# Optimization experiments

Hardware: AMD Instinct MI355X
Metric: run time of the kernel (lower is better)

Reference implementation:

```python
import jax, jax.numpy as jnp
import numpy as np

N_NODES = 100000
N_FEAT = 256
OUT_DIM = 128
NNZ_X = 1_600_000
NNZ_A = 1_600_000
DROPOUT = 0.0  # layer default; floor(1-p+u) mask is all-ones -> deterministic


def setup_inputs() -> dict:
    key = jax.random.key(0)
    k = jax.random.split(key, 7)
    feat_rows = jax.random.randint(k[0], (NNZ_X,), 0, N_NODES, dtype=jnp.int32)
    feat_cols = jax.random.randint(k[1], (NNZ_X,), 0, N_FEAT, dtype=jnp.int32)
    feat_vals = jax.random.normal(k[2], (NNZ_X,), dtype=jnp.float32)
    adj_rows = jax.random.randint(k[3], (NNZ_A,), 0, N_NODES, dtype=jnp.int32)
    adj_cols = jax.random.randint(k[4], (NNZ_A,), 0, N_NODES, dtype=jnp.int32)
    adj_vals = jax.random.uniform(k[5], (NNZ_A,), dtype=jnp.float32)
    glorot_std = np.sqrt(2.0 / (N_FEAT + OUT_DIM)).astype(np.float32)
    W = jax.random.normal(k[6], (N_FEAT, OUT_DIM), dtype=jnp.float32) * glorot_std
    return {
        "feat_rows": feat_rows, "feat_cols": feat_cols, "feat_vals": feat_vals,
        "adj_rows": adj_rows, "adj_cols": adj_cols, "adj_vals": adj_vals,
        "W": W, "n_nodes": N_NODES,
    }


def reference(feat_rows, feat_cols, feat_vals, adj_rows, adj_cols, adj_vals, W, n_nodes):
    # sparse dropout on feature nonzeros: mask = floor((1-p) + uniform) in {0,1}
    u = jax.random.uniform(jax.random.key(1), feat_vals.shape, dtype=feat_vals.dtype)
    keep = jnp.floor((1.0 - DROPOUT) + u)
    vals = feat_vals * keep * (1.0 / (1.0 - DROPOUT))
    # X @ W : gather W rows by feature column, scale by nnz value, scatter-add into node rows
    xw = jax.ops.segment_sum(vals[:, None] * W[feat_cols], feat_rows,
                             num_segments=n_nodes)  # [N, D]
    # A @ (X @ W) : gather node rows by edge source, scale by edge weight, scatter-add to dest
    agg = jax.ops.segment_sum(adj_vals[:, None] * xw[adj_cols], adj_rows,
                              num_segments=n_nodes)  # [N, D]
    return jax.nn.relu(agg)
```

## Files before the change

### kernel.cpp

```cpp
#include <hip/hip_runtime.h>
#include <hip/hip_fp16.h>

#define OUT_DIM 128
#define NPS 256
#define NS_MAX 400
#define CAP_S 4608
#define EPT2 18
#define SBLK1 256
#define EPT1 16
#define CHUNK1 (SBLK1 * EPT1)
#define SBLK2 256
#define GBLK 256

__global__ __launch_bounds__(SBLK1) void scatter1_kernel(
    const int* __restrict__ adj_rows, const int* __restrict__ adj_cols,
    const float* __restrict__ adj_vals, int nnz_a, int nCkA,
    const int* __restrict__ feat_rows, const int* __restrict__ feat_cols,
    const float* __restrict__ feat_vals, int nnz_x,
    int* __restrict__ cur, int2* __restrict__ pay, int ns)
{
    __shared__ int2 s_stage[CHUNK1];
    __shared__ unsigned short s_bin[CHUNK1];
    __shared__ int s_hist[NS_MAX];
    __shared__ int s_excl[NS_MAX];
    __shared__ int s_gbase[NS_MAX];

    int tid = threadIdx.x;
    bool isA = ((int)blockIdx.x < nCkA);
    const int* rows; const int* cols; const float* vals;
    int nnz, start, matbase;
    if (isA) {
        rows = adj_rows; cols = adj_cols; vals = adj_vals; nnz = nnz_a;
        start = (int)blockIdx.x * CHUNK1; matbase = 0;
    } else {
        rows = feat_rows; cols = feat_cols; vals = feat_vals; nnz = nnz_x;
        start = ((int)blockIdx.x - nCkA) * CHUNK1; matbase = ns;
    }
    int total = nnz - start; if (total > CHUNK1) total = CHUNK1;

    for (int i = tid; i < ns; i += SBLK1) s_hist[i] = 0;
    __syncthreads();

    int rr[EPT1]; int cc[EPT1]; float vv[EPT1];
    #pragma unroll
    for (int k = 0; k < EPT1; ++k) {
        int e = start + k * SBLK1 + tid;
        rr[k] = -1;
        if (e < nnz) {
            rr[k] = rows[e]; cc[k] = cols[e]; vv[k] = vals[e];
            atomicAdd(&s_hist[rr[k] >> 8], 1);
        }
    }
    __syncthreads();

    if (tid < 64) {
        int carry = 0;
        for (int seg = 0; seg < ns; seg += 64) {
            int idx = seg + tid;
            int x = (idx < ns) ? s_hist[idx] : 0;
            int incl = x;
            #pragma unroll
            for (int off = 1; off < 64; off <<= 1) {
                int y = __shfl_up(incl, off, 64);
                if (tid >= off) incl += y;
            }
            if (idx < ns) s_excl[idx] = carry + incl - x;
            carry += __shfl(incl, 63, 64);
        }
    }
    __syncthreads();

    for (int i = tid; i < ns; i += SBLK1) {
        int c = s_hist[i];
        s_gbase[i] = (c > 0) ? atomicAdd(&cur[matbase + i], c) : 0;
        s_hist[i] = 0;
    }
    __syncthreads();

    #pragma unroll
    for (int k = 0; k < EPT1; ++k) {
        if (rr[k] >= 0) {
            int b = rr[k] >> 8;
            int rl = rr[k] & 255;
            int pos = s_excl[b] + atomicAdd(&s_hist[b], 1);
            s_stage[pos] = make_int2((rl << 17) | cc[k], __float_as_int(vv[k]));
            s_bin[pos] = (unsigned short)b;
        }
    }
    __syncthreads();

    for (int i = tid; i < total; i += SBLK1) {
        int b = s_bin[i];
        int g = s_gbase[b] + (i - s_excl[b]);
        if (g < CAP_S)
            pay[(size_t)(matbase + b) * CAP_S + g] = s_stage[i];
    }
}

__global__ __launch_bounds__(SBLK2) void sort2_kernel(
    const int* __restrict__ cur, int2* __restrict__ pay,
    int2* __restrict__ row_span, int ns, int n_nodes)
{
    __shared__ int s_cnt[NPS];
    __shared__ int s_excl[NPS];
    int b = blockIdx.x;
    int tid = threadIdx.x;
    int count = cur[b]; if (count > CAP_S) count = CAP_S;
    int2* region = pay + (size_t)b * CAP_S;

    s_cnt[tid] = 0;
    __syncthreads();

    int2 er[EPT2];
    #pragma unroll
    for (int k = 0; k < EPT2; ++k) {
        int i = tid + k * SBLK2;
        er[k] = make_int2(-1, 0);
        if (i < count) {
            er[k] = region[i];
            atomicAdd(&s_cnt[((unsigned)er[k].x) >> 17], 1);
        }
    }
    __syncthreads();

    if (tid < 64) {
        int carry = 0;
        #pragma unroll
        for (int seg = 0; seg < NPS; seg += 64) {
            int x = s_cnt[seg + tid];
            int incl = x;
            #pragma unroll
            for (int off = 1; off < 64; off <<= 1) {
                int y = __shfl_up(incl, off, 64);
                if (tid >= off) incl += y;
            }
            s_excl[seg + tid] = carry + incl - x;
            carry += __shfl(incl, 63, 64);
        }
    }
    __syncthreads();

    int m = (b >= ns) ? 1 : 0;
    int g = (b - m * ns) * NPS + tid;
    if (g < n_nodes)
        row_span[(size_t)m * n_nodes + g] = make_int2(b * CAP_S + s_excl[tid], s_cnt[tid]);
    __syncthreads();

    #pragma unroll
    for (int k = 0; k < EPT2; ++k) {
        if (er[k].x >= 0) {
            int rl = ((unsigned)er[k].x) >> 17;
            int pos = atomicAdd(&s_excl[rl], 1);
            region[pos] = make_int2(er[k].x & 0x1FFFF, er[k].y);
        }
    }
}

__global__ __launch_bounds__(GBLK) void gather_xw_kernel(
    const int2* __restrict__ row_span, const int2* __restrict__ pay,
    const float* __restrict__ W, __half* __restrict__ XW, int n_nodes)
{
    int tid = threadIdx.x;
    int lane = tid & 15;
    int node = blockIdx.x * 16 + (tid >> 4);
    if (node >= n_nodes) return;
    int2 span = row_span[(size_t)n_nodes + node];
    int s = span.x, cnt = span.y;
    const float4* Wv = (const float4*)W;
    float a0=0,a1=0,a2=0,a3=0,a4=0,a5=0,a6=0,a7=0;
    for (int base = 0; base < cnt; base += 16) {
        int mm = cnt - base; if (mm > 16) mm = 16;
        int2 pl = make_int2(0, 0);
        if (lane < mm) pl = pay[s + base + lane];
        #pragma unroll 4
        for (int j = 0; j < mm; ++j) {
            int c = __shfl(pl.x, j, 16);
            float v = __int_as_float(__shfl(pl.y, j, 16));
            float4 f0 = Wv[c * 32 + lane * 2];
            float4 f1 = Wv[c * 32 + lane * 2 + 1];
            a0 += v * f0.x; a1 += v * f0.y; a2 += v * f0.z; a3 += v * f0.w;
            a4 += v * f1.x; a5 += v * f1.y; a6 += v * f1.z; a7 += v * f1.w;
        }
    }
    union { int4 i4; __half2 h[4]; } o;
    o.h[0] = __floats2half2_rn(a0, a1);
    o.h[1] = __floats2half2_rn(a2, a3);
    o.h[2] = __floats2half2_rn(a4, a5);
    o.h[3] = __floats2half2_rn(a6, a7);
    ((int4*)(XW + (size_t)node * OUT_DIM))[lane] = o.i4;
}

__global__ __launch_bounds__(GBLK, 4) void gather_agg_kernel(
    const int2* __restrict__ row_span, const int2* __restrict__ pay,
    const __half* __restrict__ XW, float* __restrict__ out, int n_nodes)
{
    int tid = threadIdx.x;
    int lane = tid & 15;
    int node = blockIdx.x * 16 + (tid >> 4);
    if (node >= n_nodes) return;
    int2 span = row_span[node];
    int s = span.x, cnt = span.y;
    const int4* Xv = (const int4*)XW;
    float a0=0,a1=0,a2=0,a3=0,a4=0,a5=0,a6=0,a7=0;
    int2 pl = make_int2(0, 0);
    if (lane < cnt) pl = pay[s + lane];
    for (int base = 0; base < cnt; base += 16) {
        int4 w[16];
        #pragma unroll
        for (int j = 0; j < 16; ++j) {
            int c = __shfl(pl.x, j, 16);
            w[j] = Xv[(size_t)((c << 4) | lane)];
        }
        int2 pln = make_int2(0, 0);
        if (base + 16 + lane < cnt) pln = pay[s + base + 16 + lane];
        #pragma unroll
        for (int j = 0; j < 16; ++j) {
            float v = __int_as_float(__shfl(pl.y, j, 16));
            union { int4 i4; __half2 h[4]; } u;
            u.i4 = w[j];
            float2 f0 = __half22float2(u.h[0]);
            float2 f1 = __half22float2(u.h[1]);
            float2 f2 = __half22float2(u.h[2]);
            float2 f3 = __half22float2(u.h[3]);
            a0 += v * f0.x; a1 += v * f0.y; a2 += v * f1.x; a3 += v * f1.y;
            a4 += v * f2.x; a5 += v * f2.y; a6 += v * f3.x; a7 += v * f3.y;
        }
        pl = pln;
    }
    float4 lo, hi;
    lo.x = fmaxf(a0, 0.f); lo.y = fmaxf(a1, 0.f);
    lo.z = fmaxf(a2, 0.f); lo.w = fmaxf(a3, 0.f);
    hi.x = fmaxf(a4, 0.f); hi.y = fmaxf(a5, 0.f);
    hi.z = fmaxf(a6, 0.f); hi.w = fmaxf(a7, 0.f);
    float4* orow = (float4*)(out + (size_t)node * OUT_DIM);
    orow[2 * lane]     = lo;
    orow[2 * lane + 1] = hi;
}

extern "C" void kernel_launch(void* const* d_in, const int* in_sizes, int n_in,
                              void* d_out, int out_size, void* d_ws, size_t ws_size,
                              hipStream_t stream) {
    const int*   feat_rows = (const int*)d_in[0];
    const int*   feat_cols = (const int*)d_in[1];
    const float* feat_vals = (const float*)d_in[2];
    const int*   adj_rows  = (const int*)d_in[3];
    const int*   adj_cols  = (const int*)d_in[4];
    const float* adj_vals  = (const float*)d_in[5];
    const float* W         = (const float*)d_in[6];
    float*       out       = (float*)d_out;

    const int nnz_x   = in_sizes[0];
    const int nnz_a   = in_sizes[3];
    const int n_nodes = out_size / OUT_DIM;
    const int ns      = (n_nodes + NPS - 1) / NPS;

    char* p = (char*)d_ws;
    __half* XW   = (__half*)p;  p += (size_t)n_nodes * OUT_DIM * sizeof(__half);
    p = (char*)(((uintptr_t)p + 15) & ~(uintptr_t)15);
    int2* pay    = (int2*)p;    p += (size_t)2 * ns * CAP_S * sizeof(int2);
    int2* row_span = (int2*)p;  p += (size_t)2 * n_nodes * sizeof(int2);
    int* cur     = (int*)p;     p += (size_t)2 * ns * sizeof(int);

    hipMemsetAsync(cur, 0, (size_t)2 * ns * sizeof(int), stream);

    const int nCkA = (nnz_a + CHUNK1 - 1) / CHUNK1;
    const int nCkX = (nnz_x + CHUNK1 - 1) / CHUNK1;
    scatter1_kernel<<<nCkA + nCkX, SBLK1, 0, stream>>>(
        adj_rows, adj_cols, adj_vals, nnz_a, nCkA,
        feat_rows, feat_cols, feat_vals, nnz_x,
        cur, pay, ns);

    sort2_kernel<<<2 * ns, SBLK2, 0, stream>>>(cur, pay, row_span, ns, n_nodes);

    const int gnb = (n_nodes + 15) / 16;
    gather_xw_kernel<<<gnb, GBLK, 0, stream>>>(row_span, pay, W, XW, n_nodes);
    gather_agg_kernel<<<gnb, GBLK, 0, stream>>>(row_span, pay, XW, out, n_nodes);
}
```

Before: 252.9 us.

## Densify X in fp16 and compute X@W with MFMA instead of sparse gather

```diff
diff --git a/kernel.cpp b/kernel.cpp
--- a/kernel.cpp
+++ b/kernel.cpp
@@ -2,6 +2,7 @@
 #include <hip/hip_fp16.h>
 
 #define OUT_DIM 128
+#define N_FEAT 256
 #define NPS 256
 #define NS_MAX 400
 #define CAP_S 4608
@@ -12,11 +13,84 @@
 #define SBLK2 256
 #define GBLK 256
 
+typedef _Float16 f16;
+typedef __attribute__((ext_vector_type(8))) _Float16 f16x8;
+typedef __attribute__((ext_vector_type(4))) float f32x4;
+
+__global__ __launch_bounds__(256) void scatter_x_kernel(
+    const int* __restrict__ rows, const int* __restrict__ cols,
+    const float* __restrict__ vals, int nnz, __half* __restrict__ Xd)
+{
+    int i = blockIdx.x * 256 + threadIdx.x;
+    if (i >= nnz) return;
+    int r = rows[i], c = cols[i];
+    __half hv = __float2half(vals[i]);
+    unsigned int* addr = (unsigned int*)(Xd + (size_t)r * N_FEAT + (c & ~1));
+    bool hi = (c & 1) != 0;
+    unsigned int old = *addr, assumed;
+    do {
+        assumed = old;
+        __half2 h2 = *(__half2*)&assumed;
+        if (hi) h2.y = __hadd(h2.y, hv);
+        else    h2.x = __hadd(h2.x, hv);
+        old = atomicCAS(addr, assumed, *(unsigned int*)&h2);
+    } while (old != assumed);
+}
+
+__global__ __launch_bounds__(GBLK) void gemm_xw_kernel(
+    const __half* __restrict__ Xd, const float* __restrict__ W,
+    __half* __restrict__ XW, int n_nodes)
+{
+    __shared__ __align__(16) char sWT[N_FEAT * OUT_DIM * 2];
+    int tid = threadIdx.x;
+    for (int t = tid; t < N_FEAT * OUT_DIM; t += GBLK) {
+        int c = t & 127;
+        int k = t >> 7;
+        int byte = ((c * N_FEAT + k) * 2) ^ ((c & 7) << 4);
+        *(f16*)(sWT + byte) = (f16)W[t];
+    }
+    __syncthreads();
+
+    int lane = tid & 63;
+    int wv = tid >> 6;
+    int rbase = blockIdx.x * 128 + wv * 32;
+    int lrow = lane & 15;
+    int kb = lane >> 4;
+    f32x4 acc[2][8] = {};
+    #pragma unroll
+    for (int ks = 0; ks < 8; ++ks) {
+        int k0 = ks * 32 + kb * 8;
+        f16x8 a0 = {}, a1 = {};
+        int r0 = rbase + lrow, r1 = rbase + 16 + lrow;
+        if (r0 < n_nodes) a0 = *(const f16x8*)(Xd + (size_t)r0 * N_FEAT + k0);
+        if (r1 < n_nodes) a1 = *(const f16x8*)(Xd + (size_t)r1 * N_FEAT + k0);
+        #pragma unroll
+        for (int nt = 0; nt < 8; ++nt) {
+            int c = nt * 16 + lrow;
+            int byte = ((c * N_FEAT + k0) * 2) ^ ((c & 7) << 4);
+            f16x8 b = *(const f16x8*)(sWT + byte);
+            acc[0][nt] = __builtin_amdgcn_mfma_f32_16x16x32_f16(a0, b, acc[0][nt], 0, 0, 0);
+            acc[1][nt] = __builtin_amdgcn_mfma_f32_16x16x32_f16(a1, b, acc[1][nt], 0, 0, 0);
+        }
+    }
+    #pragma unroll
+    for (int rt = 0; rt < 2; ++rt) {
+        #pragma unroll
+        for (int nt = 0; nt < 8; ++nt) {
+            #pragma unroll
+            for (int i = 0; i < 4; ++i) {
+                int r = rbase + rt * 16 + kb * 4 + i;
+                int c = nt * 16 + lrow;
+                if (r < n_nodes)
+                    XW[(size_t)r * OUT_DIM + c] = __float2half(acc[rt][nt][i]);
+            }
+        }
+    }
+}
+
 __global__ __launch_bounds__(SBLK1) void scatter1_kernel(
-    const int* __restrict__ adj_rows, const int* __restrict__ adj_cols,
-    const float* __restrict__ adj_vals, int nnz_a, int nCkA,
-    const int* __restrict__ feat_rows, const int* __restrict__ feat_cols,
-    const float* __restrict__ feat_vals, int nnz_x,
+    const int* __restrict__ rows, const int* __restrict__ cols,
+    const float* __restrict__ vals, int nnz,
     int* __restrict__ cur, int2* __restrict__ pay, int ns)
 {
     __shared__ int2 s_stage[CHUNK1];
@@ -26,16 +100,7 @@
     __shared__ int s_gbase[NS_MAX];
 
     int tid = threadIdx.x;
-    bool isA = ((int)blockIdx.x < nCkA);
-    const int* rows; const int* cols; const float* vals;
-    int nnz, start, matbase;
-    if (isA) {
-        rows = adj_rows; cols = adj_cols; vals = adj_vals; nnz = nnz_a;
-        start = (int)blockIdx.x * CHUNK1; matbase = 0;
-    } else {
-        rows = feat_rows; cols = feat_cols; vals = feat_vals; nnz = nnz_x;
-        start = ((int)blockIdx.x - nCkA) * CHUNK1; matbase = ns;
-    }
+    int start = (int)blockIdx.x * CHUNK1;
     int total = nnz - start; if (total > CHUNK1) total = CHUNK1;
 
     for (int i = tid; i < ns; i += SBLK1) s_hist[i] = 0;
@@ -72,7 +137,7 @@
 
     for (int i = tid; i < ns; i += SBLK1) {
         int c = s_hist[i];
-        s_gbase[i] = (c > 0) ? atomicAdd(&cur[matbase + i], c) : 0;
+        s_gbase[i] = (c > 0) ? atomicAdd(&cur[i], c) : 0;
         s_hist[i] = 0;
     }
     __syncthreads();
@@ -93,13 +158,13 @@
         int b = s_bin[i];
         int g = s_gbase[b] + (i - s_excl[b]);
         if (g < CAP_S)
-            pay[(size_t)(matbase + b) * CAP_S + g] = s_stage[i];
+            pay[(size_t)b * CAP_S + g] = s_stage[i];
     }
 }
 
 __global__ __launch_bounds__(SBLK2) void sort2_kernel(
     const int* __restrict__ cur, int2* __restrict__ pay,
-    int2* __restrict__ row_span, int ns, int n_nodes)
+    int2* __restrict__ row_span, int n_nodes)
 {
     __shared__ int s_cnt[NPS];
     __shared__ int s_excl[NPS];
@@ -140,10 +205,9 @@
     }
     __syncthreads();
 
-    int m = (b >= ns) ? 1 : 0;
-    int g = (b - m * ns) * NPS + tid;
+    int g = b * NPS + tid;
     if (g < n_nodes)
-        row_span[(size_t)m * n_nodes + g] = make_int2(b * CAP_S + s_excl[tid], s_cnt[tid]);
+        row_span[g] = make_int2(b * CAP_S + s_excl[tid], s_cnt[tid]);
     __syncthreads();
 
     #pragma unroll
@@ -154,40 +218,6 @@
             region[pos] = make_int2(er[k].x & 0x1FFFF, er[k].y);
         }
     }
-}
-
-__global__ __launch_bounds__(GBLK) void gather_xw_kernel(
-    const int2* __restrict__ row_span, const int2* __restrict__ pay,
-    const float* __restrict__ W, __half* __restrict__ XW, int n_nodes)
-{
-    int tid = threadIdx.x;
-    int lane = tid & 15;
-    int node = blockIdx.x * 16 + (tid >> 4);
-    if (node >= n_nodes) return;
-    int2 span = row_span[(size_t)n_nodes + node];
-    int s = span.x, cnt = span.y;
-    const float4* Wv = (const float4*)W;
-    float a0=0,a1=0,a2=0,a3=0,a4=0,a5=0,a6=0,a7=0;
-    for (int base = 0; base < cnt; base += 16) {
-        int mm = cnt - base; if (mm > 16) mm = 16;
-        int2 pl = make_int2(0, 0);
-        if (lane < mm) pl = pay[s + base + lane];
-        #pragma unroll 4
-        for (int j = 0; j < mm; ++j) {
-            int c = __shfl(pl.x, j, 16);
-            float v = __int_as_float(__shfl(pl.y, j, 16));
-            float4 f0 = Wv[c * 32 + lane * 2];
-            float4 f1 = Wv[c * 32 + lane * 2 + 1];
-            a0 += v * f0.x; a1 += v * f0.y; a2 += v * f0.z; a3 += v * f0.w;
-            a4 += v * f1.x; a5 += v * f1.y; a6 += v * f1.z; a7 += v * f1.w;
-        }
-    }
-    union { int4 i4; __half2 h[4]; } o;
-    o.h[0] = __floats2half2_rn(a0, a1);
-    o.h[1] = __floats2half2_rn(a2, a3);
-    o.h[2] = __floats2half2_rn(a4, a5);
-    o.h[3] = __floats2half2_rn(a6, a7);
-    ((int4*)(XW + (size_t)node * OUT_DIM))[lane] = o.i4;
 }
 
 __global__ __launch_bounds__(GBLK, 4) void gather_agg_kernel(
@@ -256,23 +286,25 @@
 
     char* p = (char*)d_ws;
     __half* XW   = (__half*)p;  p += (size_t)n_nodes * OUT_DIM * sizeof(__half);
+    __half* Xd   = (__half*)p;  p += (size_t)n_nodes * N_FEAT * sizeof(__half);
     p = (char*)(((uintptr_t)p + 15) & ~(uintptr_t)15);
-    int2* pay    = (int2*)p;    p += (size_t)2 * ns * CAP_S * sizeof(int2);
-    int2* row_span = (int2*)p;  p += (size_t)2 * n_nodes * sizeof(int2);
-    int* cur     = (int*)p;     p += (size_t)2 * ns * sizeof(int);
-
-    hipMemsetAsync(cur, 0, (size_t)2 * ns * sizeof(int), stream);
+    int2* pay    = (int2*)p;    p += (size_t)ns * CAP_S * sizeof(int2);
+    int2* row_span = (int2*)p;  p += (size_t)n_nodes * sizeof(int2);
+    int* cur     = (int*)p;     p += (size_t)ns * sizeof(int);
+
+    (void)hipMemsetAsync(Xd, 0, (size_t)n_nodes * N_FEAT * sizeof(__half), stream);
+    (void)hipMemsetAsync(cur, 0, (size_t)ns * sizeof(int), stream);
+
+    scatter_x_kernel<<<(nnz_x + 255) / 256, 256, 0, stream>>>(
+        feat_rows, feat_cols, feat_vals, nnz_x, Xd);
 
     const int nCkA = (nnz_a + CHUNK1 - 1) / CHUNK1;
-    const int nCkX = (nnz_x + CHUNK1 - 1) / CHUNK1;
-    scatter1_kernel<<<nCkA + nCkX, SBLK1, 0, stream>>>(
-        adj_rows, adj_cols, adj_vals, nnz_a, nCkA,
-        feat_rows, feat_cols, feat_vals, nnz_x,
-        cur, pay, ns);
-
-    sort2_kernel<<<2 * ns, SBLK2, 0, stream>>>(cur, pay, row_span, ns, n_nodes);
+    scatter1_kernel<<<nCkA, SBLK1, 0, stream>>>(
+        adj_rows, adj_cols, adj_vals, nnz_a, cur, pay, ns);
+    sort2_kernel<<<ns, SBLK2, 0, stream>>>(cur, pay, row_span, n_nodes);
+
+    gemm_xw_kernel<<<(n_nodes + 127) / 128, GBLK, 0, stream>>>(Xd, W, XW, n_nodes);
 
     const int gnb = (n_nodes + 15) / 16;
-    gather_xw_kernel<<<gnb, GBLK, 0, stream>>>(row_span, pay, W, XW, n_nodes);
     gather_agg_kernel<<<gnb, GBLK, 0, stream>>>(row_span, pay, XW, out, n_nodes);
 }
```

After: 311.8 us. +23.3%, slower.
